# Performance work log

Hardware: AMD Instinct MI355X
Metric: run time of the kernel (lower is better)

## Reference

```python
import math
import jax, jax.numpy as jnp
import numpy as np

# Frozen random shifts from the original module's __init__ (random.randint(-1,1))
SHIFT_C = 1   # p_2_0_1: roll along channel dim
SHIFT_H = 1   # p_4_1_0: roll along h
SHIFT_W = -1  # p_4_1_1: roll along w
K = 7         # horizontal window size (F.unfold kernel (1,7), padding (0,3))


def setup_inputs() -> dict:
    key = jax.random.key(0)
    k1, k2 = jax.random.split(key)
    n, c, h, w = 8, 256, 56, 56
    x = jax.random.normal(k1, (n, c, h, w), dtype=jnp.float32)
    # p_1_w ~ trunc_normal(std=0.1) around 1.0; approximate with 1 + 0.1*normal
    p1w = 1.0 + 0.1 * jax.random.normal(k2, (1, c, h, w), dtype=jnp.float32)
    return {"x": x, "p1w": p1w}


def _unfold_w7(t):
    # t: (n,c,h,w) -> (n,c,7,h,w): 7 horizontal taps, zero-padded (pad=3)
    w = t.shape[-1]
    tp = jnp.pad(t, ((0, 0), (0, 0), (0, 0), (3, 3)))
    return jnp.stack([tp[..., j:j + w] for j in range(K)], axis=2)


def reference(x, p1w):
    n, c, h, w = x.shape
    hw = h * w
    t1 = p1w * x                              # (n,c,h,w)
    t2 = jnp.roll(t1, SHIFT_C, axis=1)        # roll channels
    t3 = _unfold_w7(t2)                       # (n,c,7,h,w)
    t4 = jnp.roll(jnp.roll(t3, SHIFT_H, axis=3), SHIFT_W, axis=4)
    t5 = t1[:, :, None] - t3                  # (n,c,7,h,w)
    t6 = x[:, :, None] + t4                   # (n,c,7,h,w)
    x2 = x.reshape(n, c, hw)
    t5r = t5.reshape(n, c, K, hw)
    t6r = t6.reshape(n, c, K, hw)
    # scores: bmm(x (n,c,hw), t5^T (n,hw,c*7)) -> (n,c,c,7)
    t7 = jnp.einsum('nip,njkp->nijk', x2, t5r) / math.sqrt(hw)
    # aggregate: bmm(t7 (n,c,c*7), t6 (n,c*7,hw)) -> (n,c,hw)
    t8 = jnp.einsum('nijk,njkp->nip', t7, t6r) / math.sqrt(c * K)
    return t8.reshape(n, c, h, w)
```

## Files before the change

### kernel.cpp

```cpp
#include <hip/hip_runtime.h>

typedef unsigned short u16;
typedef __bf16 bf16x8 __attribute__((ext_vector_type(8)));
typedef float f32x4 __attribute__((ext_vector_type(4)));

#define HH  56
#define WW  56
#define HW  3136
#define CC  256
#define NB  8
#define CKP 2048
#define KS1 3

__device__ __forceinline__ u16 f2bf(float f) {
  unsigned int u = __float_as_uint(f);
  u += 0x7fffu + ((u >> 16) & 1u);
  return (u16)(u >> 16);
}
__device__ __forceinline__ float bf2f(u16 v) {
  return __uint_as_float((unsigned)v << 16);
}

__device__ __forceinline__ void lds_load16(const void* g, void* l) {
  __builtin_amdgcn_global_load_lds(
      (const __attribute__((address_space(1))) void*)g,
      (__attribute__((address_space(3))) void*)l, 16, 0, 0);
}

__global__ void pass1(const float* __restrict__ x, const float* __restrict__ p1w,
                      u16* __restrict__ t1b, u16* __restrict__ xb) {
  int i = blockIdx.x * 256 + threadIdx.x;
  int cw = i % (CC * HW / 4);
  float4 xv = ((const float4*)x)[i];
  float4 wv = ((const float4*)p1w)[cw];
  uint2 xo = make_uint2((unsigned)f2bf(xv.x) | ((unsigned)f2bf(xv.y) << 16),
                        (unsigned)f2bf(xv.z) | ((unsigned)f2bf(xv.w) << 16));
  ((uint2*)xb)[i] = xo;
  uint2 to = make_uint2((unsigned)f2bf(xv.x * wv.x) | ((unsigned)f2bf(xv.y * wv.y) << 16),
                        (unsigned)f2bf(xv.z * wv.z) | ((unsigned)f2bf(xv.w * wv.w) << 16));
  ((uint2*)t1b)[i] = to;
}

__global__ __launch_bounds__(256)
void gemm1f(const u16* __restrict__ A, const u16* __restrict__ t1b,
            float* __restrict__ Cp) {
  __shared__ u16 As0[128 * 64], As1[128 * 64];
  __shared__ u16 Bs[128 * 64];

  const int bi = blockIdx.x;
  const int nb = bi & 7;
  const int r  = bi >> 3;
  const int ks = r % 3;
  const int r2 = r / 3;
  const int m0b = r2 & 1;
  const int n0b = r2 >> 1;

  const int it0 = 49 * ks / KS1, it1 = 49 * (ks + 1) / KS1;
  const int itL = it1 - 1;
  const u16* Ab  = A   + (long)nb * CC * HW;
  const u16* t1n = t1b + (long)nb * CC * HW;
  const int m0 = m0b * 128, n0 = n0b * 128;
  const int jb = n0b * 16;
  const int t = threadIdx.x;
  const int lane = t & 63, wave = t >> 6;
  const int wm = wave & 1, wn = wave >> 1;
  const int lm = lane & 15, quad = lane >> 4;

  const int jl = (t >> 3) & 15, pc = t & 7, hf = t >> 7;
  const int j  = jb + jl;
  const int jm = (j + CC - 1) & (CC - 1);
  const u16* arow = t1n + (long)j  * HW;
  const u16* wrow = t1n + (long)jm * HW;

  f32x4 acc[4][4];
#pragma unroll
  for (int a = 0; a < 4; ++a)
#pragma unroll
    for (int b = 0; b < 4; ++b) acc[a][b] = (f32x4)0.0f;

  int rowc[4], colc[4];
#pragma unroll
  for (int ci = 0; ci < 4; ++ci) {
    int c = t + ci * 256;
    rowc[ci] = c >> 3;
    colc[ci] = ((c & 7) ^ (rowc[ci] & 7)) * 8;
  }

  __attribute__((aligned(16))) u16 ArE[8], ArO[8];
  __attribute__((aligned(16))) u16 WdE[24], WdO[24];

#define DMA1(AsD, itn) do { const int k0_ = (itn) * 64;                        \
    _Pragma("unroll")                                                          \
    for (int ci = 0; ci < 4; ++ci)                                             \
      lds_load16(Ab + (long)(m0 + rowc[ci]) * HW + k0_ + colc[ci],             \
                 &AsD[(t + ci * 256) * 8]); } while (0)

#define PF1(Ar, Wd, itn) do { const int p8_ = (itn) * 64 + pc * 8;             \
    *(uint4*)(Ar) = *(const uint4*)&arow[p8_];                                 \
    _Pragma("unroll")                                                          \
    for (int L = 0; L < 3; ++L) {                                              \
      int ad = p8_ - 8 + L * 8;                                                \
      ad = ad < 0 ? 0 : (ad > HW - 8 ? HW - 8 : ad);                           \
      *(uint4*)&(Wd)[L * 8] = *(const uint4*)&wrow[ad]; } } while (0)

#define BUILD1(Ar, Wd, itn) do {                                               \
    const int p8_ = (itn) * 64 + pc * 8;                                       \
    const int w0t_ = p8_ % 56;                                                 \
    int wvx_[8];                                                               \
    _Pragma("unroll")                                                          \
    for (int e = 0; e < 8; ++e) { int wq = w0t_ + e;                           \
      wvx_[e] = wq >= 56 ? wq - 56 : wq; }                                     \
    if (hf == 0) {                                                             \
      _Pragma("unroll")                                                        \
      for (int k = 0; k < 4; ++k) {                                            \
        __attribute__((aligned(16))) u16 v_[8];                                \
        _Pragma("unroll")                                                      \
        for (int e = 0; e < 8; ++e)                                            \
          v_[e] = ((unsigned)(wvx_[e] + k - 3) < 56u) ? (Wd)[e + k + 5] : (u16)0; \
        *(uint4*)&Bs[(jl * 8 + k) * 64 + (pc ^ k) * 8] = *(const uint4*)v_;    \
      }                                                                        \
    } else {                                                                   \
      _Pragma("unroll")                                                        \
      for (int k = 4; k < 7; ++k) {                                            \
        __attribute__((aligned(16))) u16 v_[8];                                \
        _Pragma("unroll")                                                      \
        for (int e = 0; e < 8; ++e)                                            \
          v_[e] = ((unsigned)(wvx_[e] + k - 3) < 56u) ? (Wd)[e + k + 5] : (u16)0; \
        *(uint4*)&Bs[(jl * 8 + k) * 64 + (pc ^ k) * 8] = *(const uint4*)v_;    \
      }                                                                        \
      *(uint4*)&Bs[(jl * 8 + 7) * 64 + (pc ^ 7) * 8] = *(const uint4*)(Ar);    \
    } } while (0)

#define MF1(AsS) do {                                                          \
    _Pragma("unroll")                                                          \
    for (int kk = 0; kk < 2; ++kk) {                                           \
      const int phys = ((kk * 4 + quad) ^ (lm & 7)) * 8;                       \
      bf16x8 af[4], bv[4];                                                     \
      _Pragma("unroll")                                                        \
      for (int mi = 0; mi < 4; ++mi)                                           \
        af[mi] = *(const bf16x8*)&(AsS)[(wm * 64 + mi * 16 + lm) * 64 + phys]; \
      _Pragma("unroll")                                                        \
      for (int ni = 0; ni < 4; ++ni)                                           \
        bv[ni] = *(const bf16x8*)&Bs[(wn * 64 + ni * 16 + lm) * 64 + phys];    \
      _Pragma("unroll")                                                        \
      for (int mi = 0; mi < 4; ++mi)                                           \
        _Pragma("unroll")                                                      \
        for (int ni = 0; ni < 4; ++ni)                                         \
          acc[mi][ni] = __builtin_amdgcn_mfma_f32_16x16x32_bf16(               \
              af[mi], bv[ni], acc[mi][ni], 0, 0, 0);                           \
    } } while (0)

  PF1(ArE, WdE, it0);
  DMA1(As0, it0);
  __syncthreads();
  PF1(ArO, WdO, min(it0 + 1, itL));
  BUILD1(ArE, WdE, it0);
  __syncthreads();

  int it = it0;
  while (it < it1) {
    DMA1(As1, min(it + 1, itL));
    PF1(ArE, WdE, min(it + 2, itL));
    MF1(As0);
    __syncthreads();
    BUILD1(ArO, WdO, min(it + 1, itL));
    __syncthreads();
    ++it; if (it >= it1) break;
    DMA1(As0, min(it + 1, itL));
    PF1(ArO, WdO, min(it + 2, itL));
    MF1(As1);
    __syncthreads();
    BUILD1(ArE, WdE, min(it + 1, itL));
    __syncthreads();
    ++it;
  }

#undef DMA1
#undef PF1
#undef BUILD1
#undef MF1

  float* Cb = Cp + ((long)ks * NB + nb) * (long)CC * CKP;
#pragma unroll
  for (int mi = 0; mi < 4; ++mi)
#pragma unroll
    for (int ni = 0; ni < 4; ++ni) {
      int rb = m0 + wm * 64 + mi * 16 + quad * 4;
      int cg = n0 + wn * 64 + ni * 16 + lm;
#pragma unroll
      for (int r4 = 0; r4 < 4; ++r4)
        Cb[(long)(rb + r4) * CKP + cg] = acc[mi][ni][r4];
    }
}

__global__ void reduce1(const float* __restrict__ p1, u16* __restrict__ t7) {
  const int g = blockIdx.x * 256 + threadIdx.x;
  const long S = (long)NB * CC * CKP;
  const long base = (long)g * 8;
  float a[8];
#pragma unroll
  for (int e = 0; e < 8; ++e) a[e] = 0.0f;
#pragma unroll
  for (int ks = 0; ks < KS1; ++ks) {
    float4 lo = *(const float4*)&p1[ks * S + base];
    float4 hi = *(const float4*)&p1[ks * S + base + 4];
    a[0] += lo.x; a[1] += lo.y; a[2] += lo.z; a[3] += lo.w;
    a[4] += hi.x; a[5] += hi.y; a[6] += hi.z; a[7] += hi.w;
  }
  const float s = 1.0f / 56.0f;
  const float G = a[7];
  __attribute__((aligned(16))) u16 o[8];
  float s7 = 0.0f;
#pragma unroll
  for (int k = 0; k < 7; ++k) {
    float v = (G - a[k]) * s;
    s7 += v;
    o[k] = f2bf(v);
  }
  o[7] = f2bf(s7);
  *(uint4*)&t7[base] = *(const uint4*)o;
}

__global__ __launch_bounds__(256)
void gemm2f(const u16* __restrict__ A, const u16* __restrict__ xb,
            const u16* __restrict__ t1b, float* __restrict__ out) {
  __shared__ u16 As0[128 * 64], As1[128 * 64];
  __shared__ u16 Bs0[64 * 64], Bs1[64 * 64];
  __shared__ __attribute__((aligned(16))) u16 Rs0[896], Rs1[896];

  const int bi = blockIdx.x;
  const int nb = bi & 7;
  const int r  = bi >> 3;
  const int m0b = r & 1;
  const int n0b = r >> 1;

  const u16* Ab  = A   + (long)nb * CC * CKP;
  const u16* xbn = xb  + (long)nb * CC * HW;
  const u16* t1n = t1b + (long)nb * CC * HW;
  const int m0 = m0b * 128, n0 = n0b * 64;
  const int t = threadIdx.x;
  const int lane = t & 63, wave = t >> 6;
  const int wm = wave & 1, wn = wave >> 1;
  const int lm = lane & 15, quad = lane >> 4;

  const int pr = t & 63, jg = t >> 6;
  const int p  = n0 + pr;
  const int h  = p / WW, w = p - h * WW;
  const int w2 = (w + 1) % WW;
  const int swz = pr & 7;
  const int h_lo = n0 / WW;
  const int slot = h - h_lo;

  int roff[2][7], rmsk[7];
#pragma unroll
  for (int k = 0; k < 7; ++k) {
    int ww = w2 + k - 3;
    int wc = ww < 0 ? 0 : (ww > 55 ? 55 : ww);
    rmsk[k] = ((unsigned)ww < 56u);
#pragma unroll
    for (int jj = 0; jj < 2; ++jj)
      roff[jj][k] = ((jg * 2 + jj) * 2 + slot) * 56 + wc;
  }

  long stSrcOff = 0;
  int  stCh = 0;
  bool stR = false;
  {
    if (wave == 2 || (wave == 3 && lane < 48)) {
      stR = true;
      int c = (wave == 2) ? lane : 64 + lane;
      stCh = c / 14;
      int rem = c - stCh * 14;
      int s = rem / 7, i = rem - s * 7;
      int h2s = ((h_lo + s) + HH - 1) % HH;
      stSrcOff = h2s * 56 + i * 8;
    }
  }

  f32x4 acc[4][2];
#pragma unroll
  for (int a = 0; a < 4; ++a)
#pragma unroll
    for (int b = 0; b < 2; ++b) acc[a][b] = (f32x4)0.0f;

  int rowc[4], colc[4];
#pragma unroll
  for (int ci = 0; ci < 4; ++ci) {
    int c = t + ci * 256;
    rowc[ci] = c >> 3;
    colc[ci] = ((c & 7) ^ (rowc[ci] & 7)) * 8;
  }

  u16 xrE[2], xrO[2];

#define DMAA(AsD, itn) do { const int k0_ = (itn) * 64;                        \
    _Pragma("unroll")                                                          \
    for (int ci = 0; ci < 4; ++ci)                                             \
      lds_load16(Ab + (long)(m0 + rowc[ci]) * CKP + k0_ + colc[ci],            \
                 &AsD[(t + ci * 256) * 8]); } while (0)

#define STAGE(RsD, itn) do { if (stR) {                                        \
    const int jmm_ = ((itn) * 8 + stCh + CC - 1) & (CC - 1);                   \
    lds_load16(t1n + (long)jmm_ * HW + stSrcOff,                               \
               (wave == 2) ? &RsD[lane * 8] : &RsD[512 + lane * 8]);           \
  } } while (0)

#define XPF(xr, itn) do {                                                      \
    (xr)[0] = xbn[(long)((itn) * 8 + jg * 2 + 0) * HW + p];                    \
    (xr)[1] = xbn[(long)((itn) * 8 + jg * 2 + 1) * HW + p]; } while (0)

#define BGEN(RsS, xrS, BsD) do {                                               \
    __attribute__((aligned(16))) u16 v0[8], v1[8];                             \
    _Pragma("unroll")                                                          \
    for (int k = 0; k < 7; ++k) {                                              \
      u16 a_ = (RsS)[roff[0][k]], b_ = (RsS)[roff[1][k]];                      \
      v0[k] = rmsk[k] ? a_ : (u16)0;                                           \
      v1[k] = rmsk[k] ? b_ : (u16)0;                                           \
    }                                                                          \
    v0[7] = (xrS)[0];                                                          \
    v1[7] = (xrS)[1];                                                          \
    *(uint4*)&(BsD)[pr * 64 + (((jg * 2 + 0) ^ swz) * 8)] = *(const uint4*)v0; \
    *(uint4*)&(BsD)[pr * 64 + (((jg * 2 + 1) ^ swz) * 8)] = *(const uint4*)v1; \
  } while (0)

#define MFMA2(AsS, BsS) do {                                                   \
    _Pragma("unroll")                                                          \
    for (int kk = 0; kk < 2; ++kk) {                                           \
      const int phys = ((kk * 4 + quad) ^ (lm & 7)) * 8;                       \
      bf16x8 af[4], bv[2];                                                     \
      _Pragma("unroll")                                                        \
      for (int mi = 0; mi < 4; ++mi)                                           \
        af[mi] = *(const bf16x8*)&(AsS)[(wm * 64 + mi * 16 + lm) * 64 + phys]; \
      _Pragma("unroll")                                                        \
      for (int ni = 0; ni < 2; ++ni)                                           \
        bv[ni] = *(const bf16x8*)&(BsS)[(wn * 32 + ni * 16 + lm) * 64 + phys]; \
      _Pragma("unroll")                                                        \
      for (int mi = 0; mi < 4; ++mi)                                           \
        _Pragma("unroll")                                                      \
        for (int ni = 0; ni < 2; ++ni)                                         \
          acc[mi][ni] = __builtin_amdgcn_mfma_f32_16x16x32_bf16(               \
              af[mi], bv[ni], acc[mi][ni], 0, 0, 0);                           \
    } } while (0)

  STAGE(Rs0, 0);
  XPF(xrE, 0);
  DMAA(As0, 0);
  __syncthreads();
  STAGE(Rs1, 1);
  XPF(xrO, 1);
  BGEN(Rs0, xrE, Bs0);
  __syncthreads();

  for (int itp = 0; itp < 16; ++itp) {
    const int itE = 2 * itp;
    DMAA(As1, itE + 1);
    STAGE(Rs0, min(itE + 2, 31));
    XPF(xrE, min(itE + 2, 31));
    BGEN(Rs1, xrO, Bs1);
    MFMA2(As0, Bs0);
    __syncthreads();
    DMAA(As0, min(itE + 2, 31));
    STAGE(Rs1, min(itE + 3, 31));
    XPF(xrO, min(itE + 3, 31));
    BGEN(Rs0, xrE, Bs0);
    MFMA2(As1, Bs1);
    __syncthreads();
  }

#undef DMAA
#undef STAGE
#undef XPF
#undef BGEN
#undef MFMA2

  const float s2 = 0.023622783f;
  float* Ob = out + (long)nb * CC * HW;
#pragma unroll
  for (int mi = 0; mi < 4; ++mi)
#pragma unroll
    for (int ni = 0; ni < 2; ++ni) {
      int rb = m0 + wm * 64 + mi * 16 + quad * 4;
      int cg = n0 + wn * 32 + ni * 16 + lm;
#pragma unroll
      for (int r4 = 0; r4 < 4; ++r4)
        Ob[(long)(rb + r4) * HW + cg] = acc[mi][ni][r4] * s2;
    }
}

extern "C" void kernel_launch(void* const* d_in, const int* in_sizes, int n_in,
                              void* d_out, int out_size, void* d_ws, size_t ws_size,
                              hipStream_t stream) {
  const float* x   = (const float*)d_in[0];
  const float* p1w = (const float*)d_in[1];

  char* ws = (char*)d_ws;
  size_t o = 0;
  u16* xb  = (u16*)(ws + o); o += (size_t)NB * CC * HW * 2;
  u16* t1b = (u16*)(ws + o); o += (size_t)NB * CC * HW * 2;
  u16* t7  = (u16*)(ws + o); o += (size_t)NB * CC * CKP * 2;
  float* p1 = (float*)(ws + o); o += (size_t)KS1 * NB * CC * CKP * 4;

  pass1<<<NB * CC * HW / 4 / 256, 256, 0, stream>>>(x, p1w, t1b, xb);
  gemm1f<<<NB * KS1 * 2 * 16, 256, 0, stream>>>(xb, t1b, p1);
  reduce1<<<NB * CC * CKP / 8 / 256, 256, 0, stream>>>(p1, t7);
  gemm2f<<<NB * 2 * 49, 256, 0, stream>>>(t7, xb, t1b, (float*)d_out);
}
```

Baseline: 202.7 us.

## Restructure both GEMM pipelines: single B buffer, LDS-staged x, shifted-word tap build

gemm1f goes from double-buffered A to a single A buffer with DMA and B-build inside each iteration, and its K-split count rises from 3 to 4 for more blocks. gemm2f drops one B buffer, stages the x row through LDS via async global_load_lds instead of per-thread scalar loads, and builds the 7 taps with 64-bit funnel shifts and masks instead of per-element indexed reads. The goal is less LDS footprint, higher occupancy and cheaper B-tile construction. The cost is extra barriers per iteration and less overlap between loads and MFMA.

```diff
diff --git a/kernel.cpp b/kernel.cpp
--- a/kernel.cpp
+++ b/kernel.cpp
@@ -1,6 +1,8 @@
 #include <hip/hip_runtime.h>
 
 typedef unsigned short u16;
+typedef unsigned int u32;
+typedef unsigned long long u64;
 typedef __bf16 bf16x8 __attribute__((ext_vector_type(8)));
 typedef float f32x4 __attribute__((ext_vector_type(4)));
 
@@ -10,7 +12,7 @@
 #define CC  256
 #define NB  8
 #define CKP 2048
-#define KS1 3
+#define KS1 4
 
 __device__ __forceinline__ u16 f2bf(float f) {
   unsigned int u = __float_as_uint(f);
@@ -44,19 +46,18 @@
 __global__ __launch_bounds__(256)
 void gemm1f(const u16* __restrict__ A, const u16* __restrict__ t1b,
             float* __restrict__ Cp) {
-  __shared__ u16 As0[128 * 64], As1[128 * 64];
+  __shared__ u16 As[128 * 64];
   __shared__ u16 Bs[128 * 64];
 
   const int bi = blockIdx.x;
   const int nb = bi & 7;
   const int r  = bi >> 3;
-  const int ks = r % 3;
-  const int r2 = r / 3;
+  const int ks = r & 3;
+  const int r2 = r >> 2;
   const int m0b = r2 & 1;
   const int n0b = r2 >> 1;
 
   const int it0 = 49 * ks / KS1, it1 = 49 * (ks + 1) / KS1;
-  const int itL = it1 - 1;
   const u16* Ab  = A   + (long)nb * CC * HW;
   const u16* t1n = t1b + (long)nb * CC * HW;
   const int m0 = m0b * 128, n0 = n0b * 128;
@@ -89,11 +90,11 @@
   __attribute__((aligned(16))) u16 ArE[8], ArO[8];
   __attribute__((aligned(16))) u16 WdE[24], WdO[24];
 
-#define DMA1(AsD, itn) do { const int k0_ = (itn) * 64;                        \
+#define DMA1(itn) do { const int k0_ = (itn) * 64;                             \
     _Pragma("unroll")                                                          \
     for (int ci = 0; ci < 4; ++ci)                                             \
       lds_load16(Ab + (long)(m0 + rowc[ci]) * HW + k0_ + colc[ci],             \
-                 &AsD[(t + ci * 256) * 8]); } while (0)
+                 &As[(t + ci * 256) * 8]); } while (0)
 
 #define PF1(Ar, Wd, itn) do { const int p8_ = (itn) * 64 + pc * 8;             \
     *(uint4*)(Ar) = *(const uint4*)&arow[p8_];                                 \
@@ -131,14 +132,14 @@
       *(uint4*)&Bs[(jl * 8 + 7) * 64 + (pc ^ 7) * 8] = *(const uint4*)(Ar);    \
     } } while (0)
 
-#define MF1(AsS) do {                                                          \
+#define MF1() do {                                                             \
     _Pragma("unroll")                                                          \
     for (int kk = 0; kk < 2; ++kk) {                                           \
       const int phys = ((kk * 4 + quad) ^ (lm & 7)) * 8;                       \
       bf16x8 af[4], bv[4];                                                     \
       _Pragma("unroll")                                                        \
       for (int mi = 0; mi < 4; ++mi)                                           \
-        af[mi] = *(const bf16x8*)&(AsS)[(wm * 64 + mi * 16 + lm) * 64 + phys]; \
+        af[mi] = *(const bf16x8*)&As[(wm * 64 + mi * 16 + lm) * 64 + phys];    \
       _Pragma("unroll")                                                        \
       for (int ni = 0; ni < 4; ++ni)                                           \
         bv[ni] = *(const bf16x8*)&Bs[(wn * 64 + ni * 16 + lm) * 64 + phys];    \
@@ -151,26 +152,21 @@
     } } while (0)
 
   PF1(ArE, WdE, it0);
-  DMA1(As0, it0);
-  __syncthreads();
-  PF1(ArO, WdO, min(it0 + 1, itL));
-  BUILD1(ArE, WdE, it0);
-  __syncthreads();
 
   int it = it0;
   while (it < it1) {
-    DMA1(As1, min(it + 1, itL));
-    PF1(ArE, WdE, min(it + 2, itL));
-    MF1(As0);
-    __syncthreads();
-    BUILD1(ArO, WdO, min(it + 1, itL));
+    DMA1(it);
+    BUILD1(ArE, WdE, it);
+    __syncthreads();
+    if (it + 1 < it1) PF1(ArO, WdO, it + 1);
+    MF1();
     __syncthreads();
     ++it; if (it >= it1) break;
-    DMA1(As0, min(it + 1, itL));
-    PF1(ArO, WdO, min(it + 2, itL));
-    MF1(As1);
-    __syncthreads();
-    BUILD1(ArE, WdE, min(it + 1, itL));
+    DMA1(it);
+    BUILD1(ArO, WdO, it);
+    __syncthreads();
+    if (it + 1 < it1) PF1(ArE, WdE, it + 1);
+    MF1();
     __syncthreads();
     ++it;
   }
@@ -225,8 +221,9 @@
 void gemm2f(const u16* __restrict__ A, const u16* __restrict__ xb,
             const u16* __restrict__ t1b, float* __restrict__ out) {
   __shared__ u16 As0[128 * 64], As1[128 * 64];
-  __shared__ u16 Bs0[64 * 64], Bs1[64 * 64];
-  __shared__ __attribute__((aligned(16))) u16 Rs0[896], Rs1[896];
+  __shared__ u16 Bs[64 * 64];
+  __shared__ __attribute__((aligned(16))) u16 Rs0[912], Rs1[912];
+  __shared__ __attribute__((aligned(16))) u16 Xs0[512], Xs1[512];
 
   const int bi = blockIdx.x;
   const int nb = bi & 7;
@@ -251,22 +248,33 @@
   const int h_lo = n0 / WW;
   const int slot = h - h_lo;
 
-  int roff[2][7], rmsk[7];
-#pragma unroll
-  for (int k = 0; k < 7; ++k) {
-    int ww = w2 + k - 3;
-    int wc = ww < 0 ? 0 : (ww > 55 ? 55 : ww);
-    rmsk[k] = ((unsigned)ww < 56u);
-#pragma unroll
-    for (int jj = 0; jj < 2; ++jj)
-      roff[jj][k] = ((jg * 2 + jj) * 2 + slot) * 56 + wc;
-  }
+  const int sA   = ((jg * 2 + 0) * 2 + slot) * 56 + w2 - 3;
+  const int s4   = sA & ~3;
+  const u32 sh   = (u32)(sA & 3) * 16;
+  const int b0   = 8 + s4;
+  const int b1   = b0 + 112;
+  u32 mk01, mk23, mk45, mk6;
+  {
+    u32 m[7];
+#pragma unroll
+    for (int k = 0; k < 7; ++k)
+      m[k] = ((unsigned)(w2 + k - 3) < 56u) ? 0xffffu : 0u;
+    mk01 = m[0] | (m[1] << 16);
+    mk23 = m[2] | (m[3] << 16);
+    mk45 = m[4] | (m[5] << 16);
+    mk6  = m[6];
+  }
+  const int xoff0 = (jg * 2 + 0) * 64 + pr;
+  const int xoff1 = (jg * 2 + 1) * 64 + pr;
 
   long stSrcOff = 0;
   int  stCh = 0;
-  bool stR = false;
+  bool stR = false, stX = false;
   {
-    if (wave == 2 || (wave == 3 && lane < 48)) {
+    if (wave == 1) {
+      stX = true; stCh = lane >> 3;
+      stSrcOff = n0 + (lane & 7) * 8;
+    } else if (wave == 2 || (wave == 3 && lane < 48)) {
       stR = true;
       int c = (wave == 2) ? lane : 64 + lane;
       stCh = c / 14;
@@ -291,39 +299,43 @@
     colc[ci] = ((c & 7) ^ (rowc[ci] & 7)) * 8;
   }
 
-  u16 xrE[2], xrO[2];
-
 #define DMAA(AsD, itn) do { const int k0_ = (itn) * 64;                        \
     _Pragma("unroll")                                                          \
     for (int ci = 0; ci < 4; ++ci)                                             \
       lds_load16(Ab + (long)(m0 + rowc[ci]) * CKP + k0_ + colc[ci],            \
                  &AsD[(t + ci * 256) * 8]); } while (0)
 
-#define STAGE(RsD, itn) do { if (stR) {                                        \
-    const int jmm_ = ((itn) * 8 + stCh + CC - 1) & (CC - 1);                   \
-    lds_load16(t1n + (long)jmm_ * HW + stSrcOff,                               \
-               (wave == 2) ? &RsD[lane * 8] : &RsD[512 + lane * 8]);           \
-  } } while (0)
-
-#define XPF(xr, itn) do {                                                      \
-    (xr)[0] = xbn[(long)((itn) * 8 + jg * 2 + 0) * HW + p];                    \
-    (xr)[1] = xbn[(long)((itn) * 8 + jg * 2 + 1) * HW + p]; } while (0)
-
-#define BGEN(RsS, xrS, BsD) do {                                               \
-    __attribute__((aligned(16))) u16 v0[8], v1[8];                             \
-    _Pragma("unroll")                                                          \
-    for (int k = 0; k < 7; ++k) {                                              \
-      u16 a_ = (RsS)[roff[0][k]], b_ = (RsS)[roff[1][k]];                      \
-      v0[k] = rmsk[k] ? a_ : (u16)0;                                           \
-      v1[k] = rmsk[k] ? b_ : (u16)0;                                           \
-    }                                                                          \
-    v0[7] = (xrS)[0];                                                          \
-    v1[7] = (xrS)[1];                                                          \
-    *(uint4*)&(BsD)[pr * 64 + (((jg * 2 + 0) ^ swz) * 8)] = *(const uint4*)v0; \
-    *(uint4*)&(BsD)[pr * 64 + (((jg * 2 + 1) ^ swz) * 8)] = *(const uint4*)v1; \
+#define STAGE(RsD, XsD, itn) do {                                              \
+    if (stX)                                                                   \
+      lds_load16(xbn + (long)((itn) * 8 + stCh) * HW + stSrcOff,               \
+                 &XsD[lane * 8]);                                              \
+    else if (stR) {                                                            \
+      const int jmm_ = ((itn) * 8 + stCh + CC - 1) & (CC - 1);                 \
+      lds_load16(t1n + (long)jmm_ * HW + stSrcOff,                             \
+                 (wave == 2) ? &RsD[8 + lane * 8] : &RsD[8 + 512 + lane * 8]); \
+    } } while (0)
+
+#define TAPS(RsS, bofs, xr, d4) do {                                           \
+    u64 q0 = *(const u64*)&(RsS)[(bofs)];                                      \
+    u64 q1 = *(const u64*)&(RsS)[(bofs) + 4];                                  \
+    u64 q2 = *(const u64*)&(RsS)[(bofs) + 8];                                  \
+    u64 a_ = (q0 >> sh) | (sh ? (q1 << (64u - sh)) : 0ull);                    \
+    u64 b_ = (q1 >> sh) | (sh ? (q2 << (64u - sh)) : 0ull);                    \
+    (d4) = make_uint4(((u32)a_) & mk01, ((u32)(a_ >> 32)) & mk23,              \
+                      ((u32)b_) & mk45,                                        \
+                      (((u32)(b_ >> 32)) & mk6) | ((u32)(xr) << 16));          \
   } while (0)
 
-#define MFMA2(AsS, BsS) do {                                                   \
+#define BGEN(RsS, XsS) do {                                                    \
+    u16 xr0_ = XsS[xoff0], xr1_ = XsS[xoff1];                                  \
+    uint4 d0_, d1_;                                                            \
+    TAPS(RsS, b0, xr0_, d0_);                                                  \
+    TAPS(RsS, b1, xr1_, d1_);                                                  \
+    *(uint4*)&Bs[pr * 64 + (((jg * 2 + 0) ^ swz) * 8)] = d0_;                  \
+    *(uint4*)&Bs[pr * 64 + (((jg * 2 + 1) ^ swz) * 8)] = d1_;                  \
+  } while (0)
+
+#define MFMA2(AsS) do {                                                        \
     _Pragma("unroll")                                                          \
     for (int kk = 0; kk < 2; ++kk) {                                           \
       const int phys = ((kk * 4 + quad) ^ (lm & 7)) * 8;                       \
@@ -333,7 +345,7 @@
         af[mi] = *(const bf16x8*)&(AsS)[(wm * 64 + mi * 16 + lm) * 64 + phys]; \
       _Pragma("unroll")                                                        \
       for (int ni = 0; ni < 2; ++ni)                                           \
-        bv[ni] = *(const bf16x8*)&(BsS)[(wn * 32 + ni * 16 + lm) * 64 + phys]; \
+        bv[ni] = *(const bf16x8*)&Bs[(wn * 32 + ni * 16 + lm) * 64 + phys];    \
       _Pragma("unroll")                                                        \
       for (int mi = 0; mi < 4; ++mi)                                           \
         _Pragma("unroll")                                                      \
@@ -342,34 +354,31 @@
               af[mi], bv[ni], acc[mi][ni], 0, 0, 0);                           \
     } } while (0)
 
-  STAGE(Rs0, 0);
-  XPF(xrE, 0);
+  STAGE(Rs0, Xs0, 0);
   DMAA(As0, 0);
   __syncthreads();
-  STAGE(Rs1, 1);
-  XPF(xrO, 1);
-  BGEN(Rs0, xrE, Bs0);
-  __syncthreads();
 
   for (int itp = 0; itp < 16; ++itp) {
-    const int itE = 2 * itp;
+    const int itE = itp * 2;
+    BGEN(Rs0, Xs0);
+    __syncthreads();
     DMAA(As1, itE + 1);
-    STAGE(Rs0, min(itE + 2, 31));
-    XPF(xrE, min(itE + 2, 31));
-    BGEN(Rs1, xrO, Bs1);
-    MFMA2(As0, Bs0);
-    __syncthreads();
-    DMAA(As0, min(itE + 2, 31));
-    STAGE(Rs1, min(itE + 3, 31));
-    XPF(xrO, min(itE + 3, 31));
-    BGEN(Rs0, xrE, Bs0);
-    MFMA2(As1, Bs1);
+    STAGE(Rs1, Xs1, itE + 1);
+    MFMA2(As0);
+    __syncthreads();
+    BGEN(Rs1, Xs1);
+    __syncthreads();
+    if (itE + 2 < 32) {
+      DMAA(As0, itE + 2);
+      STAGE(Rs0, Xs0, itE + 2);
+    }
+    MFMA2(As1);
     __syncthreads();
   }
 
 #undef DMAA
 #undef STAGE
-#undef XPF
+#undef TAPS
 #undef BGEN
 #undef MFMA2
 
```

New measurement: 224.3 us. 10.6% more time.
